# Kernel optimization log

Measured on AMD Instinct MI355X. Metric: run time of the kernel, lower is better.

The kernel has to match this reference:

```python
import jax, jax.numpy as jnp
import numpy as np

N = 100000   # nodes
E = 3200000  # edges (avg degree 32)
G = 512      # graphs in batch
F_IN = 10
H = 30


def setup_inputs() -> dict:
    key = jax.random.key(0)
    ks = jax.random.split(key, 14)
    x = jax.random.normal(ks[0], (N, F_IN), dtype=jnp.float32)
    edge_index = jax.random.randint(ks[1], (2, E), 0, N, dtype=jnp.int64)
    batch = jnp.sort(jax.random.randint(ks[2], (N,), 0, G, dtype=jnp.int64))
    edge_weights = jnp.ones((E,), dtype=jnp.float32)
    s = 0.1
    W1 = jax.random.normal(ks[3], (F_IN, H), jnp.float32) * s
    b1 = jnp.zeros((H,), jnp.float32)
    W2 = jax.random.normal(ks[4], (H, H), jnp.float32) * s
    b2 = jnp.zeros((H,), jnp.float32)
    W3 = jax.random.normal(ks[5], (H, H), jnp.float32) * s
    b3 = jnp.zeros((H,), jnp.float32)
    LW1 = jax.random.normal(ks[6], (H, 10), jnp.float32) * s
    Lb1 = jnp.zeros((10,), jnp.float32)
    LW2 = jax.random.normal(ks[7], (10, 2), jnp.float32) * s
    Lb2 = jnp.zeros((2,), jnp.float32)
    return dict(x=x, edge_index=edge_index, batch=batch, edge_weights=edge_weights,
                W1=W1, b1=b1, W2=W2, b2=b2, W3=W3, b3=b3,
                LW1=LW1, Lb1=Lb1, LW2=LW2, Lb2=Lb2)


def reference(x, edge_index, batch, edge_weights, W1, b1, W2, b2, W3, b3, LW1, Lb1, LW2, Lb2):
    n = x.shape[0]
    row, col = edge_index[0], edge_index[1]
    # PyG gcn_norm: add self-loops with weight 1, symmetric normalization
    loop = jnp.arange(n)
    row_f = jnp.concatenate([row, loop])
    col_f = jnp.concatenate([col, loop])
    w_f = jnp.concatenate([edge_weights, jnp.ones((n,), edge_weights.dtype)])
    deg = jax.ops.segment_sum(w_f, col_f, num_segments=n)
    dis = jnp.where(deg > 0, jax.lax.rsqrt(jnp.where(deg > 0, deg, 1.0)), 0.0)
    norm = dis[row_f] * w_f * dis[col_f]  # [E+N]

    def gcn(h, W, b):
        h = h @ W  # [N, out]
        agg = jax.ops.segment_sum(norm[:, None] * h[row_f], col_f, num_segments=n)
        return agg + b

    h = jax.nn.relu(gcn(x, W1, b1))
    h = jax.nn.relu(gcn(h, W2, b2))
    h = jax.nn.relu(gcn(h, W3, b3))  # embedding [N, 30]
    pooled = jax.ops.segment_max(h, batch, num_segments=G)  # [G, 30]
    out = jax.nn.relu(pooled @ LW1 + Lb1) @ LW2 + Lb2  # [G, 2]
    return out
```

## Files before the change

### kernel.cpp

```cpp
#include <hip/hip_runtime.h>
#include <hip/hip_bf16.h>
#include <hip/hip_fp16.h>


#define WG 256
#define CAP 9216
#define T_EDGES 16384

__global__ void k_init(int* bcur, float* pooled, int nb16, int pooledN) {
    int i = blockIdx.x * blockDim.x + threadIdx.x;
    if (i < nb16) bcur[i] = 0;
    if (i < pooledN) pooled[i] = 0.0f;
}

__global__ __launch_bounds__(1024)
void k_bucket(const int* __restrict__ row, const int* __restrict__ col,
              const float* __restrict__ w,
              int* bcur, int2* __restrict__ buck, int E, int NB) {
    __shared__ int hist[512];
    __shared__ int base[512];
    int tid = threadIdx.x;
    for (int i = tid; i < NB; i += 1024) hist[i] = 0;
    __syncthreads();
    int start = blockIdx.x * T_EDGES;
    int end = min(start + T_EDGES, E);
    for (int i = start + tid; i < end; i += 1024)
        atomicAdd(&hist[col[i] >> 8], 1);
    __syncthreads();
    for (int i = tid; i < NB; i += 1024) {
        int h = hist[i];
        base[i] = (h > 0) ? atomicAdd(&bcur[i * 16], h) : 0;
        hist[i] = 0;
    }
    __syncthreads();
    for (int i = start + tid; i < end; i += 1024) {
        int c = col[i];
        int b = c >> 8;
        int off = atomicAdd(&hist[b], 1);
        int pos = base[b] + off;
        if (pos < CAP) {
            int2 pk;
            pk.x = (c & 255) | (row[i] << 8);
            pk.y = __float_as_int(w[i]);
            buck[(size_t)b * CAP + pos] = pk;
        }
    }
}

__global__ __launch_bounds__(1024)
void k_fuse(const int* __restrict__ bcur, const int2* __restrict__ buck,
            float* __restrict__ dis, int* __restrict__ ptr,
            int2* __restrict__ csr, int N, int NB) {
    __shared__ int lc[256];
    __shared__ float lw[256];
    __shared__ int sh[256];
    __shared__ int cur[256];
    __shared__ int sb[512];
    int b = blockIdx.x;
    int tid = threadIdx.x;
    if (tid < 512) sb[tid] = (tid < NB) ? min(bcur[tid * 16], CAP) : 0;
    if (tid < 256) { lc[tid] = 0; lw[tid] = 0.0f; }
    __syncthreads();
    for (int off = 1; off < 512; off <<= 1) {
        int v = (tid < 512 && tid >= off) ? sb[tid - off] : 0;
        __syncthreads();
        if (tid < 512) sb[tid] += v;
        __syncthreads();
    }
    int m = min(bcur[b * 16], CAP);
    int bbase = sb[b] - m;
    if (b == 0 && tid == 0) ptr[N] = sb[511];
    const int2* bp = buck + (size_t)b * CAP;
    for (int i = tid; i < m; i += 1024) {
        int2 pk = bp[i];
        int lcol = pk.x & 255;
        atomicAdd(&lc[lcol], 1);
        atomicAdd(&lw[lcol], __int_as_float(pk.y));
    }
    __syncthreads();
    int lcnt = 0;
    if (tid < 256) { lcnt = lc[tid]; sh[tid] = lcnt; }
    __syncthreads();
    for (int off = 1; off < 256; off <<= 1) {
        int t = (tid >= off && tid < 256) ? sh[tid - off] : 0;
        __syncthreads();
        if (tid < 256) sh[tid] += t;
        __syncthreads();
    }
    int node = (b << 8) + tid;
    if (tid < 256) {
        int base = bbase + sh[tid] - lcnt;
        cur[tid] = base;
        if (node < N) {
            ptr[node] = base;
            float d = 1.0f + lw[tid];
            dis[node] = (d > 0.0f) ? (1.0f / sqrtf(d)) : 0.0f;
        }
    }
    __syncthreads();
    for (int i = tid; i < m; i += 1024) {
        int2 pk = bp[i];
        int lcol = pk.x & 255;
        int pos = atomicAdd(&cur[lcol], 1);
        int2 rec;
        rec.x = (int)(((unsigned)pk.x) >> 8);
        rec.y = pk.y;
        csr[pos] = rec;
    }
}

__global__ void k_stage(const float* __restrict__ x, const float* __restrict__ dis,
                        __half* __restrict__ xp, int n) {
    int gid = blockIdx.x * blockDim.x + threadIdx.x;
    int node = gid >> 4, f = gid & 15;
    if (node < n)
        xp[(size_t)node * 16 + f] = __float2half((f < 10) ? dis[node] * x[(size_t)node * 10 + f] : 0.0f);
}

__global__ __launch_bounds__(256, 4)
void k_agg16(const __half* __restrict__ xp, const float* __restrict__ dis,
             const int* __restrict__ ptr, const int2* __restrict__ csr,
             float* __restrict__ y, int n) {
    int wid = (blockIdx.x * blockDim.x + threadIdx.x) >> 6;
    int lane = threadIdx.x & 63;
    int f = lane & 15;
    int laneq = lane & 48;
    int node = 4 * wid + (lane >> 4);
    bool valid = node < n;
    int s = 0, e = 0;
    if (valid) { s = ptr[node]; e = ptr[node + 1]; }
    int len = e - s;
    int m01 = max(__shfl(len, 0, 64), __shfl(len, 16, 64));
    int m23 = max(__shfl(len, 32, 64), __shfl(len, 48, 64));
    int maxlen = max(m01, m23);
    float a0 = 0.0f, a1 = 0.0f, a2 = 0.0f, a3 = 0.0f;
    for (int off = 0; off < maxlen; off += 16) {
        int idxv = 0; float nrmv = 0.0f;
        if (off + f < len) {
            int2 v = csr[s + off + f];
            idxv = v.x;
            nrmv = __int_as_float(v.y);
        }
        float wt[16], vt[16];
#pragma unroll
        for (int j = 0; j < 16; j++) {
            int r = __shfl(idxv, laneq | j, 64);
            wt[j] = __shfl(nrmv, laneq | j, 64);
            vt[j] = __half2float(xp[(size_t)r * 16 + f]);
        }
#pragma unroll
        for (int j = 0; j < 16; j += 4) {
            a0 = fmaf(wt[j],     vt[j],     a0);
            a1 = fmaf(wt[j + 1], vt[j + 1], a1);
            a2 = fmaf(wt[j + 2], vt[j + 2], a2);
            a3 = fmaf(wt[j + 3], vt[j + 3], a3);
        }
    }
    if (valid) {
        float acc = (a0 + a1) + (a2 + a3);
        float r = dis[node] * (acc + __half2float(xp[(size_t)node * 16 + f]));
        y[(size_t)node * 16 + f] = r;
    }
}

__global__ __launch_bounds__(256)
void k_lin1(const float* __restrict__ y, const float* __restrict__ W1,
            const float* __restrict__ b1, const float* __restrict__ W2,
            const float* __restrict__ dis, __half* __restrict__ out, int n) {
    __shared__ float W1s[10 * 32];
    __shared__ float W2s[30 * 32];
    __shared__ float b1s[32];
    __shared__ float ys[8][16];
    __shared__ float hs[8][32];
    int tid = threadIdx.x;
    for (int i = tid; i < 10 * 32; i += 256) { int k = i >> 5, f = i & 31; W1s[i] = (f < 30) ? W1[k * 30 + f] : 0.0f; }
    for (int i = tid; i < 30 * 32; i += 256) { int k = i >> 5, f = i & 31; W2s[i] = (f < 30) ? W2[k * 30 + f] : 0.0f; }
    if (tid < 32) b1s[tid] = (tid < 30) ? b1[tid] : 0.0f;
    int n8 = tid >> 5, f = tid & 31;
    int node = blockIdx.x * 8 + n8;
    __syncthreads();
    if (node < n && f < 16) ys[n8][f] = y[(size_t)node * 16 + f];
    __syncthreads();
    if (node < n) {
        float h = b1s[f];
#pragma unroll
        for (int k = 0; k < 10; k++) h += ys[n8][k] * W1s[k * 32 + f];
        h = fmaxf(h, 0.0f);
        if (f >= 30) h = 0.0f;
        hs[n8][f] = h;
    }
    __syncthreads();
    if (node < n) {
        float o = 0.0f;
#pragma unroll
        for (int k = 0; k < 30; k++) o += hs[n8][k] * W2s[k * 32 + f];
        out[(size_t)node * 32 + f] = __float2half(o * dis[node]);
    }
}

__global__ void k_matmul30(const float* __restrict__ in,
                           const float* __restrict__ W, const float* __restrict__ dis,
                           __half* __restrict__ out, int n) {
    __shared__ float Ws[30 * 30];
    for (int idx = threadIdx.x; idx < 30 * 30; idx += blockDim.x) Ws[idx] = W[idx];
    __syncthreads();
    int gid = blockIdx.x * blockDim.x + threadIdx.x;
    int node = gid >> 5;
    int f = gid & 31;
    if (node < n) {
        float acc = 0.0f;
        if (f < 30) {
            const float* ip = in + (size_t)node * 32;
#pragma unroll
            for (int k = 0; k < 30; k++) acc += ip[k] * Ws[k * 30 + f];
            acc *= dis[node];
        }
        out[(size_t)node * 32 + f] = __float2half(acc);
    }
}

__global__ __launch_bounds__(256, 4)
void k_agg(const __half* __restrict__ hw, const float* __restrict__ dis,
           const int* __restrict__ ptr, const int2* __restrict__ csr,
           const float* __restrict__ bias, const int* __restrict__ batch,
           float* __restrict__ out, float* __restrict__ pooled, int n) {
    int wid = (blockIdx.x * blockDim.x + threadIdx.x) >> 6;
    int lane = threadIdx.x & 63;
    if (wid >= n) return;
    int f = lane & 31;
    int half = lane >> 5;
    int s = ptr[wid];
    int e = ptr[wid + 1];
    float a0 = 0.0f, a1 = 0.0f, a2 = 0.0f, a3 = 0.0f;
    for (int base = s; base < e; base += 32) {
        int idxv = 0; float nrmv = 0.0f;
        int src = base + lane;
        if (lane < 32 && src < e) {
            int2 v = csr[src];
            idxv = v.x;
            nrmv = __int_as_float(v.y);
        }
        float wt[16], vt[16];
#pragma unroll
        for (int j = 0; j < 16; j++) {
            int sl = 2 * j + half;
            int r = __shfl(idxv, sl, 64);
            wt[j] = __shfl(nrmv, sl, 64);
            vt[j] = __half2float(hw[(size_t)r * 32 + f]);
        }
#pragma unroll
        for (int j = 0; j < 16; j += 4) {
            a0 = fmaf(wt[j],     vt[j],     a0);
            a1 = fmaf(wt[j + 1], vt[j + 1], a1);
            a2 = fmaf(wt[j + 2], vt[j + 2], a2);
            a3 = fmaf(wt[j + 3], vt[j + 3], a3);
        }
    }
    float acc = (a0 + a1) + (a2 + a3);
    acc += __shfl_xor(acc, 32, 64);
    float dc = dis[wid];
    float r = dc * (acc + __half2float(hw[(size_t)wid * 32 + f]));
    if (half == 0 && f < 30) {
        r = fmaxf(r + bias[f], 0.0f);
        if (pooled) {
            int g = batch[wid];
            atomicMax((int*)&pooled[g * 32 + f], __float_as_int(r));
        } else {
            out[(size_t)wid * 32 + f] = r;
        }
    }
}

__global__ void k_mlp(const float* __restrict__ pooled,
                      const float* __restrict__ LW1, const float* __restrict__ Lb1,
                      const float* __restrict__ LW2, const float* __restrict__ Lb2,
                      float* __restrict__ out, int G) {
    int g = blockIdx.x * blockDim.x + threadIdx.x;
    if (g >= G) return;
    float p[30];
#pragma unroll
    for (int k = 0; k < 30; k++) p[k] = pooled[g * 32 + k];
    float o0 = Lb2[0], o1 = Lb2[1];
#pragma unroll
    for (int j = 0; j < 10; j++) {
        float hj = Lb1[j];
#pragma unroll
        for (int k = 0; k < 30; k++) hj += p[k] * LW1[k * 10 + j];
        hj = fmaxf(hj, 0.0f);
        o0 += hj * LW2[j * 2 + 0];
        o1 += hj * LW2[j * 2 + 1];
    }
    out[g * 2 + 0] = o0;
    out[g * 2 + 1] = o1;
}

extern "C" void kernel_launch(void* const* d_in, const int* in_sizes, int n_in,
                              void* d_out, int out_size, void* d_ws, size_t ws_size,
                              hipStream_t stream) {
    const float* x     = (const float*)d_in[0];
    const int*   ei    = (const int*)d_in[1];
    const int*   batch = (const int*)d_in[2];
    const float* ew    = (const float*)d_in[3];
    const float* W1 = (const float*)d_in[4];  const float* b1  = (const float*)d_in[5];
    const float* W2 = (const float*)d_in[6];  const float* b2  = (const float*)d_in[7];
    const float* W3 = (const float*)d_in[8];  const float* b3  = (const float*)d_in[9];
    const float* LW1 = (const float*)d_in[10]; const float* Lb1 = (const float*)d_in[11];
    const float* LW2 = (const float*)d_in[12]; const float* Lb2 = (const float*)d_in[13];
    float* out = (float*)d_out;

    const int N = in_sizes[2];
    const int E = in_sizes[3];
    const int G = out_size / 2;
    const int* row = ei;
    const int* col = ei + E;

    const int NB = (N + 255) >> 8;

    char* p = (char*)d_ws;
    auto carve = [&](size_t bytes) -> void* {
        void* r = (void*)p;
        p += (bytes + 255) & ~(size_t)255;
        return r;
    };
    int*   ptr       = (int*)carve((size_t)(N + 1) * 4);
    float* dis       = (float*)carve((size_t)N * 4);
    int*   bcur      = (int*)carve((size_t)NB * 16 * 4);
    int2*  csr       = (int2*)carve((size_t)E * 8);
    size_t buckBytes = (size_t)NB * CAP * 8;
    size_t featBytes = (size_t)N * 32 * 4 * 2;
    char*  regionA   = (char*)carve(buckBytes > featBytes ? buckBytes : featBytes);
    int2*  buck      = (int2*)regionA;
    float* bufA      = (float*)regionA;
    __half* xp       = (__half*)regionA;
    float* y16       = (float*)(regionA + (size_t)N * 16 * 2);
    __half* bufB     = (__half*)(regionA + (size_t)N * 32 * 4);
    float* pooled    = (float*)carve((size_t)G * 32 * 4);

    int initN = (NB * 16 > G * 32) ? NB * 16 : G * 32;

    k_init<<<(initN + WG - 1) / WG, WG, 0, stream>>>(bcur, pooled, NB * 16, G * 32);
    k_bucket<<<(E + T_EDGES - 1) / T_EDGES, 1024, 0, stream>>>(row, col, ew, bcur, buck, E, NB);
    k_fuse<<<NB, 1024, 0, stream>>>(bcur, buck, dis, ptr, csr, N, NB);

    int agg_grid   = (int)(((size_t)N * 64 + WG - 1) / WG);
    int agg16_grid = (int)(((size_t)((N + 3) / 4) * 64 + WG - 1) / WG);
    int mm_grid    = (int)(((size_t)N * 32 + WG - 1) / WG);

    k_stage<<<(int)(((size_t)N * 16 + WG - 1) / WG), WG, 0, stream>>>(x, dis, xp, N);
    k_agg16<<<agg16_grid, WG, 0, stream>>>(xp, dis, ptr, csr, y16, N);
    k_lin1<<<(N + 7) / 8, 256, 0, stream>>>(y16, W1, b1, W2, dis, bufB, N);
    k_agg<<<agg_grid, WG, 0, stream>>>(bufB, dis, ptr, csr, b2, batch, bufA, nullptr, N);
    k_matmul30<<<mm_grid, WG, 0, stream>>>(bufA, W3, dis, bufB, N);
    k_agg<<<agg_grid, WG, 0, stream>>>(bufB, dis, ptr, csr, b3, batch, nullptr, pooled, N);

    k_mlp<<<(G + WG - 1) / WG, WG, 0, stream>>>(pooled, LW1, Lb1, LW2, Lb2, out, G);
}
```

Before: 396.8 us.

## Split CSR by source-node half to localize gathers in aggregation kernels

Partitions each destination's edge list into two segments by whether the source row is in the lower or upper half of nodes, with separate pointer arrays. The 30-wide aggregation now runs as two interleaved partial passes, each gathering only from one half of the feature table so the working set fits better in cache. The partial sums are combined later in the matmul and in a new combine-and-pool kernel that also reduces max-pooling atomics per block. This adds an extra histogram and scan in the CSR build, doubles the partial-output traffic, and adds one more kernel launch.

```diff
diff --git a/kernel.cpp b/kernel.cpp
--- a/kernel.cpp
+++ b/kernel.cpp
@@ -7,30 +7,37 @@
 #define CAP 9216
 #define T_EDGES 16384
 
-__global__ void k_init(int* bcur, float* pooled, int nb16, int pooledN) {
+__global__ void k_init(int* bcur, float* pooled, int nb32, int pooledN) {
     int i = blockIdx.x * blockDim.x + threadIdx.x;
-    if (i < nb16) bcur[i] = 0;
+    if (i < nb32) bcur[i] = 0;
     if (i < pooledN) pooled[i] = 0.0f;
 }
 
 __global__ __launch_bounds__(1024)
 void k_bucket(const int* __restrict__ row, const int* __restrict__ col,
               const float* __restrict__ w,
-              int* bcur, int2* __restrict__ buck, int E, int NB) {
+              int* bcur, int* bcurA, int2* __restrict__ buck,
+              int E, int NB, int NHALF) {
     __shared__ int hist[512];
+    __shared__ int histA[512];
     __shared__ int base[512];
     int tid = threadIdx.x;
-    for (int i = tid; i < NB; i += 1024) hist[i] = 0;
+    for (int i = tid; i < NB; i += 1024) { hist[i] = 0; histA[i] = 0; }
     __syncthreads();
     int start = blockIdx.x * T_EDGES;
     int end = min(start + T_EDGES, E);
-    for (int i = start + tid; i < end; i += 1024)
-        atomicAdd(&hist[col[i] >> 8], 1);
+    for (int i = start + tid; i < end; i += 1024) {
+        int b = col[i] >> 8;
+        atomicAdd(&hist[b], 1);
+        if (row[i] < NHALF) atomicAdd(&histA[b], 1);
+    }
     __syncthreads();
     for (int i = tid; i < NB; i += 1024) {
         int h = hist[i];
         base[i] = (h > 0) ? atomicAdd(&bcur[i * 16], h) : 0;
-        hist[i] = 0;
+        int hA = histA[i];
+        if (hA > 0) atomicAdd(&bcurA[i * 16], hA);
+        hist[i] = 0; histA[i] = 0;
     }
     __syncthreads();
     for (int i = start + tid; i < end; i += 1024) {
@@ -48,18 +55,22 @@
 }
 
 __global__ __launch_bounds__(1024)
-void k_fuse(const int* __restrict__ bcur, const int2* __restrict__ buck,
-            float* __restrict__ dis, int* __restrict__ ptr,
-            int2* __restrict__ csr, int N, int NB) {
-    __shared__ int lc[256];
+void k_fuse(const int* __restrict__ bcur, const int* __restrict__ bcurA,
+            const int2* __restrict__ buck,
+            float* __restrict__ dis, int* __restrict__ ptrA, int* __restrict__ ptrB,
+            int2* __restrict__ csr, int N, int NB, int NHALF) {
+    __shared__ int lcA[256];
+    __shared__ int lcB[256];
     __shared__ float lw[256];
-    __shared__ int sh[256];
-    __shared__ int cur[256];
+    __shared__ int shA[256];
+    __shared__ int shB[256];
+    __shared__ int curA[256];
+    __shared__ int curB[256];
     __shared__ int sb[512];
     int b = blockIdx.x;
     int tid = threadIdx.x;
-    if (tid < 512) sb[tid] = (tid < NB) ? min(bcur[tid * 16], CAP) : 0;
-    if (tid < 256) { lc[tid] = 0; lw[tid] = 0.0f; }
+    if (tid < 512) sb[tid] = (tid < NB) ? min(bcurA[tid * 16], CAP) : 0;
+    if (tid < 256) { lcA[tid] = 0; lcB[tid] = 0; lw[tid] = 0.0f; }
     __syncthreads();
     for (int off = 1; off < 512; off <<= 1) {
         int v = (tid < 512 && tid >= off) ? sb[tid - off] : 0;
@@ -67,43 +78,63 @@
         if (tid < 512) sb[tid] += v;
         __syncthreads();
     }
-    int m = min(bcur[b * 16], CAP);
-    int bbase = sb[b] - m;
-    if (b == 0 && tid == 0) ptr[N] = sb[511];
+    int mA = min(bcurA[b * 16], CAP);
+    int bbaseA = sb[b] - mA;
+    int sumA = sb[511];
+    __syncthreads();
+    if (tid < 512) sb[tid] = (tid < NB) ? min(bcur[tid * 16], CAP) : 0;
+    __syncthreads();
+    for (int off = 1; off < 512; off <<= 1) {
+        int v = (tid < 512 && tid >= off) ? sb[tid - off] : 0;
+        __syncthreads();
+        if (tid < 512) sb[tid] += v;
+        __syncthreads();
+    }
+    int mT = min(bcur[b * 16], CAP);
+    int bbaseT = sb[b] - mT;
+    int sumT = sb[511];
+    int bbaseB = sumA + (bbaseT - bbaseA);
+    if (b == 0 && tid == 0) { ptrA[N] = sumA; ptrB[N] = sumT; }
     const int2* bp = buck + (size_t)b * CAP;
-    for (int i = tid; i < m; i += 1024) {
+    for (int i = tid; i < mT; i += 1024) {
         int2 pk = bp[i];
         int lcol = pk.x & 255;
-        atomicAdd(&lc[lcol], 1);
+        int rw = (int)(((unsigned)pk.x) >> 8);
+        if (rw < NHALF) atomicAdd(&lcA[lcol], 1); else atomicAdd(&lcB[lcol], 1);
         atomicAdd(&lw[lcol], __int_as_float(pk.y));
     }
     __syncthreads();
-    int lcnt = 0;
-    if (tid < 256) { lcnt = lc[tid]; sh[tid] = lcnt; }
+    int lcntA = 0, lcntB = 0;
+    if (tid < 256) { lcntA = lcA[tid]; shA[tid] = lcntA; lcntB = lcB[tid]; shB[tid] = lcntB; }
     __syncthreads();
     for (int off = 1; off < 256; off <<= 1) {
-        int t = (tid >= off && tid < 256) ? sh[tid - off] : 0;
-        __syncthreads();
-        if (tid < 256) sh[tid] += t;
+        int tA = (tid >= off && tid < 256) ? shA[tid - off] : 0;
+        int tB = (tid >= off && tid < 256) ? shB[tid - off] : 0;
+        __syncthreads();
+        if (tid < 256) { shA[tid] += tA; shB[tid] += tB; }
         __syncthreads();
     }
     int node = (b << 8) + tid;
     if (tid < 256) {
-        int base = bbase + sh[tid] - lcnt;
-        cur[tid] = base;
+        int baseA = bbaseA + shA[tid] - lcntA;
+        int baseB = bbaseB + shB[tid] - lcntB;
+        curA[tid] = baseA;
+        curB[tid] = baseB;
         if (node < N) {
-            ptr[node] = base;
+            ptrA[node] = baseA;
+            ptrB[node] = baseB;
             float d = 1.0f + lw[tid];
             dis[node] = (d > 0.0f) ? (1.0f / sqrtf(d)) : 0.0f;
         }
     }
     __syncthreads();
-    for (int i = tid; i < m; i += 1024) {
+    for (int i = tid; i < mT; i += 1024) {
         int2 pk = bp[i];
         int lcol = pk.x & 255;
-        int pos = atomicAdd(&cur[lcol], 1);
+        int rw = (int)(((unsigned)pk.x) >> 8);
+        int pos = atomicAdd((rw < NHALF) ? &curA[lcol] : &curB[lcol], 1);
         int2 rec;
-        rec.x = (int)(((unsigned)pk.x) >> 8);
+        rec.x = rw;
         rec.y = pk.y;
         csr[pos] = rec;
     }
@@ -119,7 +150,8 @@
 
 __global__ __launch_bounds__(256, 4)
 void k_agg16(const __half* __restrict__ xp, const float* __restrict__ dis,
-             const int* __restrict__ ptr, const int2* __restrict__ csr,
+             const int* __restrict__ ptrA, const int* __restrict__ ptrB,
+             const int2* __restrict__ csr,
              float* __restrict__ y, int n) {
     int wid = (blockIdx.x * blockDim.x + threadIdx.x) >> 6;
     int lane = threadIdx.x & 63;
@@ -127,33 +159,36 @@
     int laneq = lane & 48;
     int node = 4 * wid + (lane >> 4);
     bool valid = node < n;
-    int s = 0, e = 0;
-    if (valid) { s = ptr[node]; e = ptr[node + 1]; }
-    int len = e - s;
-    int m01 = max(__shfl(len, 0, 64), __shfl(len, 16, 64));
-    int m23 = max(__shfl(len, 32, 64), __shfl(len, 48, 64));
-    int maxlen = max(m01, m23);
     float a0 = 0.0f, a1 = 0.0f, a2 = 0.0f, a3 = 0.0f;
-    for (int off = 0; off < maxlen; off += 16) {
-        int idxv = 0; float nrmv = 0.0f;
-        if (off + f < len) {
-            int2 v = csr[s + off + f];
-            idxv = v.x;
-            nrmv = __int_as_float(v.y);
-        }
-        float wt[16], vt[16];
-#pragma unroll
-        for (int j = 0; j < 16; j++) {
-            int r = __shfl(idxv, laneq | j, 64);
-            wt[j] = __shfl(nrmv, laneq | j, 64);
-            vt[j] = __half2float(xp[(size_t)r * 16 + f]);
-        }
-#pragma unroll
-        for (int j = 0; j < 16; j += 4) {
-            a0 = fmaf(wt[j],     vt[j],     a0);
-            a1 = fmaf(wt[j + 1], vt[j + 1], a1);
-            a2 = fmaf(wt[j + 2], vt[j + 2], a2);
-            a3 = fmaf(wt[j + 3], vt[j + 3], a3);
+    for (int pass = 0; pass < 2; ++pass) {
+        const int* P = pass ? ptrB : ptrA;
+        int s = 0, e = 0;
+        if (valid) { s = P[node]; e = P[node + 1]; }
+        int len = e - s;
+        int m01 = max(__shfl(len, 0, 64), __shfl(len, 16, 64));
+        int m23 = max(__shfl(len, 32, 64), __shfl(len, 48, 64));
+        int maxlen = max(m01, m23);
+        for (int off = 0; off < maxlen; off += 16) {
+            int idxv = 0; float nrmv = 0.0f;
+            if (off + f < len) {
+                int2 v = csr[s + off + f];
+                idxv = v.x;
+                nrmv = __int_as_float(v.y);
+            }
+            float wt[16], vt[16];
+#pragma unroll
+            for (int j = 0; j < 16; j++) {
+                int r = __shfl(idxv, laneq | j, 64);
+                wt[j] = __shfl(nrmv, laneq | j, 64);
+                vt[j] = __half2float(xp[(size_t)r * 16 + f]);
+            }
+#pragma unroll
+            for (int j = 0; j < 16; j += 4) {
+                a0 = fmaf(wt[j],     vt[j],     a0);
+                a1 = fmaf(wt[j + 1], vt[j + 1], a1);
+                a2 = fmaf(wt[j + 2], vt[j + 2], a2);
+                a3 = fmaf(wt[j + 3], vt[j + 3], a3);
+            }
         }
     }
     if (valid) {
@@ -198,39 +233,24 @@
     }
 }
 
-__global__ void k_matmul30(const float* __restrict__ in,
-                           const float* __restrict__ W, const float* __restrict__ dis,
-                           __half* __restrict__ out, int n) {
-    __shared__ float Ws[30 * 30];
-    for (int idx = threadIdx.x; idx < 30 * 30; idx += blockDim.x) Ws[idx] = W[idx];
-    __syncthreads();
-    int gid = blockIdx.x * blockDim.x + threadIdx.x;
-    int node = gid >> 5;
-    int f = gid & 31;
-    if (node < n) {
-        float acc = 0.0f;
-        if (f < 30) {
-            const float* ip = in + (size_t)node * 32;
-#pragma unroll
-            for (int k = 0; k < 30; k++) acc += ip[k] * Ws[k * 30 + f];
-            acc *= dis[node];
-        }
-        out[(size_t)node * 32 + f] = __float2half(acc);
-    }
-}
-
 __global__ __launch_bounds__(256, 4)
-void k_agg(const __half* __restrict__ hw, const float* __restrict__ dis,
-           const int* __restrict__ ptr, const int2* __restrict__ csr,
-           const float* __restrict__ bias, const int* __restrict__ batch,
-           float* __restrict__ out, float* __restrict__ pooled, int n) {
-    int wid = (blockIdx.x * blockDim.x + threadIdx.x) >> 6;
+void k_agg_part(const __half* __restrict__ hw, const float* __restrict__ dis,
+                const int* __restrict__ ptrA, const int* __restrict__ ptrB,
+                const int2* __restrict__ csr,
+                float* __restrict__ pA, float* __restrict__ pB,
+                int n, int C, int NHALF) {
+    int bid = blockIdx.x;
+    int half = bid & 1;
+    int chunk = (bid >> 3) * 4 + ((bid & 7) >> 1);
+    if (chunk >= C) return;
+    int node = chunk * 4 + (threadIdx.x >> 6);
+    if (node >= n) return;
     int lane = threadIdx.x & 63;
-    if (wid >= n) return;
     int f = lane & 31;
-    int half = lane >> 5;
-    int s = ptr[wid];
-    int e = ptr[wid + 1];
+    int hlane = lane >> 5;
+    const int* P = half ? ptrB : ptrA;
+    int s = P[node];
+    int e = P[node + 1];
     float a0 = 0.0f, a1 = 0.0f, a2 = 0.0f, a3 = 0.0f;
     for (int base = s; base < e; base += 32) {
         int idxv = 0; float nrmv = 0.0f;
@@ -243,7 +263,7 @@
         float wt[16], vt[16];
 #pragma unroll
         for (int j = 0; j < 16; j++) {
-            int sl = 2 * j + half;
+            int sl = 2 * j + hlane;
             int r = __shfl(idxv, sl, 64);
             wt[j] = __shfl(nrmv, sl, 64);
             vt[j] = __half2float(hw[(size_t)r * 32 + f]);
@@ -258,15 +278,74 @@
     }
     float acc = (a0 + a1) + (a2 + a3);
     acc += __shfl_xor(acc, 32, 64);
-    float dc = dis[wid];
-    float r = dc * (acc + __half2float(hw[(size_t)wid * 32 + f]));
-    if (half == 0 && f < 30) {
-        r = fmaxf(r + bias[f], 0.0f);
-        if (pooled) {
-            int g = batch[wid];
-            atomicMax((int*)&pooled[g * 32 + f], __float_as_int(r));
+    bool selfHere = (node < NHALF) == (half == 0);
+    if (hlane == 0 && f < 30) {
+        float selfv = selfHere ? __half2float(hw[(size_t)node * 32 + f]) : 0.0f;
+        float r = dis[node] * (acc + selfv);
+        float* out = half ? pB : pA;
+        out[(size_t)node * 32 + f] = r;
+    }
+}
+
+__global__ void k_matmul30(const float* __restrict__ in0, const float* __restrict__ in1,
+                           const float* __restrict__ bias,
+                           const float* __restrict__ W, const float* __restrict__ dis,
+                           __half* __restrict__ out, int n) {
+    __shared__ float Ws[30 * 30];
+    __shared__ float bs[32];
+    for (int idx = threadIdx.x; idx < 30 * 30; idx += blockDim.x) Ws[idx] = W[idx];
+    if (threadIdx.x < 32) bs[threadIdx.x] = (threadIdx.x < 30) ? bias[threadIdx.x] : 0.0f;
+    __syncthreads();
+    int gid = blockIdx.x * blockDim.x + threadIdx.x;
+    int node = gid >> 5;
+    int f = gid & 31;
+    if (node < n) {
+        float acc = 0.0f;
+        if (f < 30) {
+            const float* p0 = in0 + (size_t)node * 32;
+            const float* p1 = in1 + (size_t)node * 32;
+#pragma unroll
+            for (int k = 0; k < 30; k++) {
+                float h = fmaxf(p0[k] + p1[k] + bs[k], 0.0f);
+                acc += h * Ws[k * 30 + f];
+            }
+            acc *= dis[node];
+        }
+        out[(size_t)node * 32 + f] = __float2half(acc);
+    }
+}
+
+__global__ __launch_bounds__(256)
+void k_combine_pool(const float* __restrict__ pA, const float* __restrict__ pB,
+                    const float* __restrict__ bias, const int* __restrict__ batch,
+                    float* __restrict__ pooled, int n) {
+    __shared__ float red[8][32];
+    __shared__ int grp[8];
+    int tid = threadIdx.x;
+    int n8 = tid >> 5, f = tid & 31;
+    int node = blockIdx.x * 8 + n8;
+    float v = 0.0f;
+    bool valid = (node < n) && (f < 30);
+    if (valid)
+        v = fmaxf(pA[(size_t)node * 32 + f] + pB[(size_t)node * 32 + f] + bias[f], 0.0f);
+    red[n8][f] = v;
+    if (f == 0) grp[n8] = (node < n) ? batch[node] : -1;
+    __syncthreads();
+    if (tid < 32 && tid < 30) {
+        int g0 = grp[0];
+        bool same = (g0 >= 0);
+        for (int k = 1; k < 8; k++) same = same && (grp[k] == g0);
+        if (same) {
+            float m = red[0][tid];
+#pragma unroll
+            for (int k = 1; k < 8; k++) m = fmaxf(m, red[k][tid]);
+            atomicMax((int*)&pooled[g0 * 32 + tid], __float_as_int(m));
         } else {
-            out[(size_t)wid * 32 + f] = r;
+            for (int k = 0; k < 8; k++) {
+                int g = grp[k];
+                if (g >= 0)
+                    atomicMax((int*)&pooled[g * 32 + tid], __float_as_int(red[k][tid]));
+            }
         }
     }
 }
@@ -311,6 +390,7 @@
     const int N = in_sizes[2];
     const int E = in_sizes[3];
     const int G = out_size / 2;
+    const int NHALF = N >> 1;
     const int* row = ei;
     const int* col = ei + E;
 
@@ -322,36 +402,41 @@
         p += (bytes + 255) & ~(size_t)255;
         return r;
     };
-    int*   ptr       = (int*)carve((size_t)(N + 1) * 4);
+    int*   ptrA      = (int*)carve((size_t)(N + 1) * 4);
+    int*   ptrB      = (int*)carve((size_t)(N + 1) * 4);
     float* dis       = (float*)carve((size_t)N * 4);
-    int*   bcur      = (int*)carve((size_t)NB * 16 * 4);
+    int*   bcur      = (int*)carve((size_t)NB * 16 * 4 * 2);
+    int*   bcurA     = bcur + (size_t)NB * 16;
     int2*  csr       = (int2*)carve((size_t)E * 8);
     size_t buckBytes = (size_t)NB * CAP * 8;
-    size_t featBytes = (size_t)N * 32 * 4 * 2;
+    size_t featBytes = (size_t)N * 32 * 4 * 2 + (size_t)N * 32 * 2;
     char*  regionA   = (char*)carve(buckBytes > featBytes ? buckBytes : featBytes);
     int2*  buck      = (int2*)regionA;
-    float* bufA      = (float*)regionA;
+    float* pA        = (float*)regionA;
+    float* pB        = (float*)(regionA + (size_t)N * 32 * 4);
+    __half* bufB     = (__half*)(regionA + (size_t)N * 32 * 4 * 2);
     __half* xp       = (__half*)regionA;
     float* y16       = (float*)(regionA + (size_t)N * 16 * 2);
-    __half* bufB     = (__half*)(regionA + (size_t)N * 32 * 4);
     float* pooled    = (float*)carve((size_t)G * 32 * 4);
 
-    int initN = (NB * 16 > G * 32) ? NB * 16 : G * 32;
-
-    k_init<<<(initN + WG - 1) / WG, WG, 0, stream>>>(bcur, pooled, NB * 16, G * 32);
-    k_bucket<<<(E + T_EDGES - 1) / T_EDGES, 1024, 0, stream>>>(row, col, ew, bcur, buck, E, NB);
-    k_fuse<<<NB, 1024, 0, stream>>>(bcur, buck, dis, ptr, csr, N, NB);
-
-    int agg_grid   = (int)(((size_t)N * 64 + WG - 1) / WG);
+    int initN = (NB * 32 > G * 32) ? NB * 32 : G * 32;
+
+    k_init<<<(initN + WG - 1) / WG, WG, 0, stream>>>(bcur, pooled, NB * 32, G * 32);
+    k_bucket<<<(E + T_EDGES - 1) / T_EDGES, 1024, 0, stream>>>(row, col, ew, bcur, bcurA, buck, E, NB, NHALF);
+    k_fuse<<<NB, 1024, 0, stream>>>(bcur, bcurA, buck, dis, ptrA, ptrB, csr, N, NB, NHALF);
+
     int agg16_grid = (int)(((size_t)((N + 3) / 4) * 64 + WG - 1) / WG);
     int mm_grid    = (int)(((size_t)N * 32 + WG - 1) / WG);
+    const int C    = (N + 3) / 4;
+    int aggp_grid  = ((C + 3) / 4) * 8;
 
     k_stage<<<(int)(((size_t)N * 16 + WG - 1) / WG), WG, 0, stream>>>(x, dis, xp, N);
-    k_agg16<<<agg16_grid, WG, 0, stream>>>(xp, dis, ptr, csr, y16, N);
+    k_agg16<<<agg16_grid, WG, 0, stream>>>(xp, dis, ptrA, ptrB, csr, y16, N);
     k_lin1<<<(N + 7) / 8, 256, 0, stream>>>(y16, W1, b1, W2, dis, bufB, N);
-    k_agg<<<agg_grid, WG, 0, stream>>>(bufB, dis, ptr, csr, b2, batch, bufA, nullptr, N);
-    k_matmul30<<<mm_grid, WG, 0, stream>>>(bufA, W3, dis, bufB, N);
-    k_agg<<<agg_grid, WG, 0, stream>>>(bufB, dis, ptr, csr, b3, batch, nullptr, pooled, N);
+    k_agg_part<<<aggp_grid, WG, 0, stream>>>(bufB, dis, ptrA, ptrB, csr, pA, pB, N, C, NHALF);
+    k_matmul30<<<mm_grid, WG, 0, stream>>>(pA, pB, b2, W3, dis, bufB, N);
+    k_agg_part<<<aggp_grid, WG, 0, stream>>>(bufB, dis, ptrA, ptrB, csr, pA, pB, N, C, NHALF);
+    k_combine_pool<<<(N + 7) / 8, 256, 0, stream>>>(pA, pB, b3, batch, pooled, N);
 
     k_mlp<<<(G + WG - 1) / WG, WG, 0, stream>>>(pooled, LW1, Lb1, LW2, Lb2, out, G);
 }
```

After: 450.9 us. 13.6% more time.
